# Kernel optimization log

Measured on AMD Instinct MI355X. Metric: run time of the kernel, lower is better.

## Reference

```python
import jax, jax.numpy as jnp
import numpy as np

N_HEAD = 16
RMS_EPS = 1.1920928955078125e-07  # torch float32 finfo eps (F.rms_norm default)


def _apply_rotary(x, cos, sin):
    # x: [B,T,H,D], cos/sin: [1,T,1,D/2]
    d = x.shape[-1] // 2
    x1, x2 = x[..., :d], x[..., d:]
    return jnp.concatenate([x1 * cos + x2 * sin, -x1 * sin + x2 * cos], axis=-1)


def _rms_norm(x):
    var = jnp.mean(jnp.square(x), axis=-1, keepdims=True)
    return x * jax.lax.rsqrt(var + RMS_EPS)


def setup_inputs() -> dict:
    key = jax.random.key(0)
    ks = jax.random.split(key, 5)
    B, T, C, H = 2, 2048, 1024, N_HEAD
    D = C // H
    x = jax.random.normal(ks[0], (B, T, C), dtype=jnp.float32)
    cos = jax.random.uniform(ks[1], (1, T, 1, D // 2), dtype=jnp.float32)
    sin = jax.random.uniform(ks[2], (1, T, 1, D // 2), dtype=jnp.float32)
    kv_w = jax.random.normal(ks[3], (C, C), dtype=jnp.float32) * (C ** -0.5)
    proj_w = jax.random.normal(ks[4], (C, C), dtype=jnp.float32) * (C ** -0.5)
    return {"x": x, "cos": cos, "sin": sin, "kv_w": kv_w, "proj_w": proj_w, "window_left": 1024}


def reference(x, cos, sin, kv_w, proj_w, window_left):
    B, T, C = x.shape
    H = N_HEAD
    D = C // H
    scale = D ** -0.5

    q = x.reshape(B, T, H, D)                       # no Q projection
    kv = (x @ kv_w.T).reshape(B, T, H, D)           # tied K=V projection

    q = _rms_norm(_apply_rotary(q, cos, sin))
    kv = _rms_norm(_apply_rotary(kv, cos, sin))

    # scores: [B,H,T,T]
    scores = jnp.einsum('bqhd,bkhd->bhqk', q, kv) * scale

    pos = jnp.arange(T)
    dist = pos[:, None] - pos[None, :]              # query_pos - key_pos
    allowed = (dist >= 0) & (dist <= window_left)   # causal + sliding window
    scores = jnp.where(allowed[None, None], scores, -jnp.inf)

    attn = jax.nn.softmax(scores, axis=-1)
    out = jnp.einsum('bhqk,bkhd->bqhd', attn, kv).reshape(B, T, C)
    return out @ proj_w.T
```

## Files before the change

kernel.cpp:

```cpp
#include <hip/hip_runtime.h>
#include <hip/hip_bf16.h>

using u16 = unsigned short;
typedef __attribute__((ext_vector_type(8))) short short8v;
typedef __attribute__((ext_vector_type(4))) float f32x4;

#define MFMA16(a, b, c) __builtin_amdgcn_mfma_f32_16x16x32_bf16((a), (b), (c), 0, 0, 0)

#define GLOAD16(g, l) __builtin_amdgcn_global_load_lds(                       \
    (const __attribute__((address_space(1))) void*)(const void*)(g),          \
    (__attribute__((address_space(3))) void*)(void*)(l), 16, 0, 0)

static __device__ __forceinline__ u16 f2bf(float x) {
  __hip_bfloat16 h = __float2bfloat16(x);
  return __builtin_bit_cast(u16, h);
}

__global__ __launch_bounds__(256) void cast3_f32_bf16(const float* __restrict__ a, u16* __restrict__ da,
                                                      const float* __restrict__ b, u16* __restrict__ db,
                                                      const float* __restrict__ c, u16* __restrict__ dc) {
  int bid = blockIdx.x;
  const float* s; u16* d; int i;
  if (bid < 4096)      { s = a; d = da; i = bid; }
  else if (bid < 5120) { s = b; d = db; i = bid - 4096; }
  else                 { s = c; d = dc; i = bid - 5120; }
  int idx = (i * 256 + threadIdx.x) * 4;
  float4 v = *reinterpret_cast<const float4*>(s + idx);
  ushort4 o;
  o.x = f2bf(v.x); o.y = f2bf(v.y); o.z = f2bf(v.z); o.w = f2bf(v.w);
  *reinterpret_cast<ushort4*>(d + idx) = o;
}

__global__ __launch_bounds__(256) void gemm_bt(const u16* __restrict__ A,
                                               const u16* __restrict__ Bt,
                                               float* __restrict__ C,
                                               int M, int N, int K) {
  __shared__ u16 As[4][64 * 32];
  __shared__ u16 Bs[4][128 * 32];
  unsigned flat = blockIdx.y * gridDim.x + blockIdx.x;
  unsigned nwg = gridDim.x * gridDim.y;
  unsigned swz = (flat & 7) * (nwg >> 3) + (flat >> 3);
  int bm = swz % gridDim.x, bn = swz / gridDim.x;
  int tid = threadIdx.x;
  int wid = tid >> 6, l = tid & 63, lr = l & 15, lg = l >> 4;
  int wr = wid >> 1, wc = wid & 1;

  int srow = l >> 2, scol = (l & 3) * 8;
  const u16* Ag  = A  + (size_t)(bm * 64 + wid * 16 + srow) * K + scol;
  const u16* Bg0 = Bt + (size_t)(bn * 128 + wid * 32 + srow) * K + scol;
  const u16* Bg1 = Bg0 + (size_t)16 * K;

  f32x4 acc[2][4];
#pragma unroll
  for (int m = 0; m < 2; m++)
#pragma unroll
    for (int n = 0; n < 4; n++) acc[m][n] = (f32x4){0.f, 0.f, 0.f, 0.f};

  const int NT = K >> 5;

#pragma unroll
  for (int t = 0; t < 2; t++) {
    GLOAD16(Ag + t * 32, &As[t][wid * 512]);
    GLOAD16(Bg0 + t * 32, &Bs[t][wid * 1024]);
    GLOAD16(Bg1 + t * 32, &Bs[t][wid * 1024 + 512]);
  }

  for (int t = 0; t < NT; t++) {
    int cur = t & 3;
    if (t + 2 < NT) {
      int nb = (t + 2) & 3;
      int ko = (t + 2) * 32;
      GLOAD16(Ag + ko, &As[nb][wid * 512]);
      GLOAD16(Bg0 + ko, &Bs[nb][wid * 1024]);
      GLOAD16(Bg1 + ko, &Bs[nb][wid * 1024 + 512]);
    }
    if (t + 2 < NT)      asm volatile("s_waitcnt vmcnt(6)" ::: "memory");
    else if (t + 1 < NT) asm volatile("s_waitcnt vmcnt(3)" ::: "memory");
    else                 asm volatile("s_waitcnt vmcnt(0)" ::: "memory");
    __builtin_amdgcn_s_barrier();

    short8v af[2], bfr[4];
#pragma unroll
    for (int m = 0; m < 2; m++)
      af[m] = *reinterpret_cast<const short8v*>(&As[cur][(wr * 32 + m * 16 + lr) * 32 + lg * 8]);
#pragma unroll
    for (int n = 0; n < 4; n++)
      bfr[n] = *reinterpret_cast<const short8v*>(&Bs[cur][(wc * 64 + n * 16 + lr) * 32 + lg * 8]);
    asm volatile("s_waitcnt lgkmcnt(0)" ::: "memory");
    __builtin_amdgcn_sched_barrier(0);
    __builtin_amdgcn_s_setprio(1);
#pragma unroll
    for (int m = 0; m < 2; m++)
#pragma unroll
      for (int n = 0; n < 4; n++) acc[m][n] = MFMA16(af[m], bfr[n], acc[m][n]);
    __builtin_amdgcn_s_setprio(0);
  }

#pragma unroll
  for (int m = 0; m < 2; m++)
#pragma unroll
    for (int n = 0; n < 4; n++)
#pragma unroll
      for (int r = 0; r < 4; r++) {
        int row = bm * 64 + wr * 32 + m * 16 + lg * 4 + r;
        int col = bn * 128 + wc * 64 + n * 16 + lr;
        C[(size_t)row * N + col] = acc[m][n][r];
      }
}

__global__ __launch_bounds__(256) void rope_rms(const float* __restrict__ src,
                                                u16* __restrict__ dst,
                                                const float* __restrict__ cosp,
                                                const float* __restrict__ sinp,
                                                float scale) {
  int R = blockIdx.x * 4 + (threadIdx.x >> 6);
  int l = threadIdx.x & 63;
  int h = R & 15;
  int bt = R >> 4;
  int t = bt & 2047, b = bt >> 11;

  float v = src[((size_t)R << 6) + l];
  float p = __shfl_xor(v, 32);
  float c = cosp[(t << 5) + (l & 31)];
  float s = sinp[(t << 5) + (l & 31)];
  float r = v * c + ((l < 32) ? p * s : -p * s);
  float sq = r * r;
  sq += __shfl_xor(sq, 32);
  sq += __shfl_xor(sq, 16);
  sq += __shfl_xor(sq, 8);
  sq += __shfl_xor(sq, 4);
  sq += __shfl_xor(sq, 2);
  sq += __shfl_xor(sq, 1);
  float inv = rsqrtf(sq * (1.0f / 64.0f) + 1.1920928955078125e-07f) * scale;
  dst[((((size_t)b * 16 + h) * 2048 + t) << 6) + l] = f2bf(r * inv);
}

__global__ __launch_bounds__(256) void transpose_td(const u16* __restrict__ src,
                                                    u16* __restrict__ dst) {
  __shared__ u16 Ld[64][72];
  int t0 = blockIdx.x << 6, bh = blockIdx.y;
  int tid = threadIdx.x;
#pragma unroll
  for (int i = 0; i < 2; i++) {
    int c = tid + i * 256, tr = c >> 3, sg = c & 7;
    *reinterpret_cast<short8v*>(&Ld[tr][sg * 8]) =
        *reinterpret_cast<const short8v*>(src + ((size_t)bh * 2048 + t0 + tr) * 64 + sg * 8);
  }
  __syncthreads();
#pragma unroll
  for (int i = 0; i < 2; i++) {
    int c = tid + i * 256, dr = c >> 3, sg = c & 7;
    short8v v;
#pragma unroll
    for (int j = 0; j < 8; j++) v[j] = (short)Ld[sg * 8 + j][dr];
    *reinterpret_cast<short8v*>(dst + ((size_t)bh * 64 + dr) * 2048 + t0 + sg * 8) = v;
  }
}

__global__ __launch_bounds__(256) void attn_swa(const u16* __restrict__ Q,
                                                const u16* __restrict__ KV,
                                                const u16* __restrict__ KVt,
                                                u16* __restrict__ O,
                                                const int* __restrict__ winp) {
  const int T = 2048;
  int bid = blockIdx.x;
  int bh = bid & 31;
  int qi = 31 - (bid >> 5);
  int q0 = qi << 6;
  int b = bh >> 4, h = bh & 15;
  int W = *winp;
  int tid = threadIdx.x;
  int wid = tid >> 6, l = tid & 63, lr = l & 15, lg = l >> 4;

  __shared__ u16 Kl[64][72];
  __shared__ u16 Vt[64][72];
  __shared__ u16 Pl[4][16][72];

  const u16* Qb = Q + (((size_t)bh * T + q0 + wid * 16 + lr) << 6);
  short8v aq0 = *reinterpret_cast<const short8v*>(Qb + lg * 8);
  short8v aq1 = *reinterpret_cast<const short8v*>(Qb + 32 + lg * 8);

  const short one_bf = (short)0x3F80;
  short8v vones = {one_bf, one_bf, one_bf, one_bf, one_bf, one_bf, one_bf, one_bf};

  float m_run[4], l_run[4];
  f32x4 oacc[4];
#pragma unroll
  for (int r = 0; r < 4; r++) { m_run[r] = -1e30f; l_run[r] = 0.f; }
#pragma unroll
  for (int dt = 0; dt < 4; dt++) oacc[dt] = (f32x4){0.f, 0.f, 0.f, 0.f};

  int lo = q0 - W;
  if (lo < 0) lo = 0;
  lo &= ~63;

  const u16* KVbh  = KV + (((size_t)bh * T) << 6);
  const u16* KVtbh = KVt + ((size_t)bh << 6) * T;
  int r8 = tid >> 3, sg = tid & 7;

  short8v vK0 = *reinterpret_cast<const short8v*>(KVbh + ((size_t)(lo + r8) << 6) + sg * 8);
  short8v vK1 = *reinterpret_cast<const short8v*>(KVbh + ((size_t)(lo + r8 + 32) << 6) + sg * 8);
  short8v vV0 = *reinterpret_cast<const short8v*>(KVtbh + (size_t)r8 * T + lo + sg * 8);
  short8v vV1 = *reinterpret_cast<const short8v*>(KVtbh + (size_t)(r8 + 32) * T + lo + sg * 8);

  for (int kt = lo; kt <= q0; kt += 64) {
    __syncthreads();
    *reinterpret_cast<short8v*>(&Kl[r8][sg * 8]) = vK0;
    *reinterpret_cast<short8v*>(&Kl[r8 + 32][sg * 8]) = vK1;
    *reinterpret_cast<short8v*>(&Vt[r8][sg * 8]) = vV0;
    *reinterpret_cast<short8v*>(&Vt[r8 + 32][sg * 8]) = vV1;
    __syncthreads();
    if (kt < q0) {
      vK0 = *reinterpret_cast<const short8v*>(KVbh + ((size_t)(kt + 64 + r8) << 6) + sg * 8);
      vK1 = *reinterpret_cast<const short8v*>(KVbh + ((size_t)(kt + 64 + r8 + 32) << 6) + sg * 8);
      vV0 = *reinterpret_cast<const short8v*>(KVtbh + (size_t)r8 * T + kt + 64 + sg * 8);
      vV1 = *reinterpret_cast<const short8v*>(KVtbh + (size_t)(r8 + 32) * T + kt + 64 + sg * 8);
    }

    f32x4 s[4];
    __builtin_amdgcn_s_setprio(1);
#pragma unroll
    for (int nt = 0; nt < 4; nt++) {
      s[nt] = (f32x4){0.f, 0.f, 0.f, 0.f};
      short8v b0 = *reinterpret_cast<const short8v*>(&Kl[nt * 16 + lr][lg * 8]);
      s[nt] = MFMA16(aq0, b0, s[nt]);
      short8v b1 = *reinterpret_cast<const short8v*>(&Kl[nt * 16 + lr][32 + lg * 8]);
      s[nt] = MFMA16(aq1, b1, s[nt]);
    }
    __builtin_amdgcn_s_setprio(0);

    bool edge = (kt + 63 > q0 + wid * 16) || ((q0 - kt) + wid * 16 + 15 > W);

    float al4[4];
#pragma unroll
    for (int r = 0; r < 4; r++) {
      float sv[4], mt;
      if (edge) {
        int t = q0 + wid * 16 + lg * 4 + r;
        mt = -3e38f;
#pragma unroll
        for (int nt = 0; nt < 4; nt++) {
          int k = kt + nt * 16 + lr;
          float val = ((k <= t) && (t - k <= W)) ? s[nt][r] : -3e38f;
          sv[nt] = val;
          mt = fmaxf(mt, val);
        }
      } else {
#pragma unroll
        for (int nt = 0; nt < 4; nt++) sv[nt] = s[nt][r];
        mt = fmaxf(fmaxf(sv[0], sv[1]), fmaxf(sv[2], sv[3]));
      }
      mt = fmaxf(mt, __shfl_xor(mt, 1));
      mt = fmaxf(mt, __shfl_xor(mt, 2));
      mt = fmaxf(mt, __shfl_xor(mt, 4));
      mt = fmaxf(mt, __shfl_xor(mt, 8));
      float mn = fmaxf(m_run[r], mt);
      float al = exp2f(m_run[r] - mn);
      m_run[r] = mn;
      al4[r] = al;
#pragma unroll
      for (int nt = 0; nt < 4; nt++) {
        Pl[wid][lg * 4 + r][nt * 16 + lr] = f2bf(exp2f(sv[nt] - mn));
      }
#pragma unroll
      for (int dt = 0; dt < 4; dt++) oacc[dt][r] *= al;
    }

    short8v ap0 = *reinterpret_cast<const short8v*>(&Pl[wid][lr][lg * 8]);
    short8v ap1 = *reinterpret_cast<const short8v*>(&Pl[wid][lr][32 + lg * 8]);
    f32x4 psum = (f32x4){0.f, 0.f, 0.f, 0.f};
    __builtin_amdgcn_s_setprio(1);
    psum = MFMA16(ap0, vones, psum);
    psum = MFMA16(ap1, vones, psum);
#pragma unroll
    for (int dt = 0; dt < 4; dt++) {
      short8v v0 = *reinterpret_cast<const short8v*>(&Vt[dt * 16 + lr][lg * 8]);
      oacc[dt] = MFMA16(ap0, v0, oacc[dt]);
      short8v v1 = *reinterpret_cast<const short8v*>(&Vt[dt * 16 + lr][32 + lg * 8]);
      oacc[dt] = MFMA16(ap1, v1, oacc[dt]);
    }
    __builtin_amdgcn_s_setprio(0);
#pragma unroll
    for (int r = 0; r < 4; r++) l_run[r] = l_run[r] * al4[r] + psum[r];
  }

#pragma unroll
  for (int r = 0; r < 4; r++) {
    int t = q0 + wid * 16 + lg * 4 + r;
    float inv = 1.f / l_run[r];
#pragma unroll
    for (int dt = 0; dt < 4; dt++) {
      O[(((size_t)b * T + t) << 10) + (h << 6) + dt * 16 + lr] = f2bf(oacc[dt][r] * inv);
    }
  }
}

extern "C" void kernel_launch(void* const* d_in, const int* in_sizes, int n_in,
                              void* d_out, int out_size, void* d_ws, size_t ws_size,
                              hipStream_t stream) {
  (void)in_sizes; (void)n_in; (void)out_size; (void)ws_size;
  const float* x    = (const float*)d_in[0];
  const float* cosp = (const float*)d_in[1];
  const float* sinp = (const float*)d_in[2];
  const float* kvw  = (const float*)d_in[3];
  const float* pw   = (const float*)d_in[4];
  const int*   win  = (const int*)d_in[5];

  char* w = (char*)d_ws;
  u16*   xbf   = (u16*)(w);
  u16*   kvwbf = (u16*)(w + (8u << 20));
  u16*   pwbf  = (u16*)(w + (10u << 20));
  float* kvf   = (float*)(w + (12u << 20));
  u16*   kvt   = (u16*)(w + (12u << 20));
  u16*   aout  = (u16*)(w + (20u << 20));
  u16*   kvbf  = (u16*)(w + (28u << 20));
  u16*   qbf   = xbf;

  cast3_f32_bf16<<<6144, 256, 0, stream>>>(x, xbf, kvw, kvwbf, pw, pwbf);

  gemm_bt<<<dim3(64, 8), 256, 0, stream>>>(xbf, kvwbf, kvf, 4096, 1024, 1024);

  rope_rms<<<16384, 256, 0, stream>>>(x, qbf, cosp, sinp, 0.18033688011112042f);
  rope_rms<<<16384, 256, 0, stream>>>(kvf, kvbf, cosp, sinp, 1.0f);

  transpose_td<<<dim3(32, 32), 256, 0, stream>>>(kvbf, kvt);

  attn_swa<<<1024, 256, 0, stream>>>(qbf, kvbf, kvt, aout, win);

  gemm_bt<<<dim3(64, 8), 256, 0, stream>>>(aout, pwbf, (float*)d_out, 4096, 1024, 1024);
}
```

Measured before the change: 201.4 us.

## Fuse KV rope/rmsnorm with transpose and drop online-softmax max tracking

Merges the KV rope+RMSnorm pass and the transpose kernel into one kernel that writes both the row-major and transposed bf16 KV, removing one launch and a round trip through global memory. In attention, the running max and rescaling are replaced by a fixed offset of 12 in exp2. This works because q and kv are RMS-normalized, so scaled scores are bounded (|s| ≤ 8·log2e·... ≈ 11.5). It also removes the setprio hints. The fixed offset relies on that norm bound to keep exp2 from overflowing or underflowing in bf16 and fp32.

Result: faster. 180.8 us (-10.2%).

```diff
diff --git a/kernel.cpp b/kernel.cpp
--- a/kernel.cpp
+++ b/kernel.cpp
@@ -135,16 +135,38 @@
   dst[((((size_t)b * 16 + h) * 2048 + t) << 6) + l] = f2bf(r * inv);
 }
 
-__global__ __launch_bounds__(256) void transpose_td(const u16* __restrict__ src,
-                                                    u16* __restrict__ dst) {
+__global__ __launch_bounds__(256) void rope_rms_kv(const float* __restrict__ src,
+                                                   u16* __restrict__ dst,
+                                                   u16* __restrict__ dstT,
+                                                   const float* __restrict__ cosp,
+                                                   const float* __restrict__ sinp) {
   __shared__ u16 Ld[64][72];
-  int t0 = blockIdx.x << 6, bh = blockIdx.y;
+  int t0 = blockIdx.x << 6;
+  int bh = blockIdx.y;
+  int b = bh >> 4, h = bh & 15;
   int tid = threadIdx.x;
-#pragma unroll
-  for (int i = 0; i < 2; i++) {
-    int c = tid + i * 256, tr = c >> 3, sg = c & 7;
-    *reinterpret_cast<short8v*>(&Ld[tr][sg * 8]) =
-        *reinterpret_cast<const short8v*>(src + ((size_t)bh * 2048 + t0 + tr) * 64 + sg * 8);
+  int w = tid >> 6, l = tid & 63;
+
+  float cl, sl;
+  for (int i = 0; i < 16; i++) {
+    int tt = w * 16 + i;
+    int t = t0 + tt;
+    float v = src[((((size_t)b * 2048 + t) * 16 + h) << 6) + l];
+    float p = __shfl_xor(v, 32);
+    cl = cosp[(t << 5) + (l & 31)];
+    sl = sinp[(t << 5) + (l & 31)];
+    float r = v * cl + ((l < 32) ? p * sl : -p * sl);
+    float sq = r * r;
+    sq += __shfl_xor(sq, 32);
+    sq += __shfl_xor(sq, 16);
+    sq += __shfl_xor(sq, 8);
+    sq += __shfl_xor(sq, 4);
+    sq += __shfl_xor(sq, 2);
+    sq += __shfl_xor(sq, 1);
+    float inv = rsqrtf(sq * (1.0f / 64.0f) + 1.1920928955078125e-07f);
+    u16 val = f2bf(r * inv);
+    dst[(((size_t)bh * 2048 + t) << 6) + l] = val;
+    Ld[tt][l] = val;
   }
   __syncthreads();
 #pragma unroll
@@ -153,7 +175,7 @@
     short8v v;
 #pragma unroll
     for (int j = 0; j < 8; j++) v[j] = (short)Ld[sg * 8 + j][dr];
-    *reinterpret_cast<short8v*>(dst + ((size_t)bh * 64 + dr) * 2048 + t0 + sg * 8) = v;
+    *reinterpret_cast<short8v*>(dstT + ((size_t)bh * 64 + dr) * 2048 + t0 + sg * 8) = v;
   }
 }
 
@@ -183,10 +205,10 @@
   const short one_bf = (short)0x3F80;
   short8v vones = {one_bf, one_bf, one_bf, one_bf, one_bf, one_bf, one_bf, one_bf};
 
-  float m_run[4], l_run[4];
+  float l_run[4];
   f32x4 oacc[4];
 #pragma unroll
-  for (int r = 0; r < 4; r++) { m_run[r] = -1e30f; l_run[r] = 0.f; }
+  for (int r = 0; r < 4; r++) l_run[r] = 0.f;
 #pragma unroll
   for (int dt = 0; dt < 4; dt++) oacc[dt] = (f32x4){0.f, 0.f, 0.f, 0.f};
 
@@ -218,7 +240,6 @@
     }
 
     f32x4 s[4];
-    __builtin_amdgcn_s_setprio(1);
 #pragma unroll
     for (int nt = 0; nt < 4; nt++) {
       s[nt] = (f32x4){0.f, 0.f, 0.f, 0.f};
@@ -227,49 +248,28 @@
       short8v b1 = *reinterpret_cast<const short8v*>(&Kl[nt * 16 + lr][32 + lg * 8]);
       s[nt] = MFMA16(aq1, b1, s[nt]);
     }
-    __builtin_amdgcn_s_setprio(0);
 
     bool edge = (kt + 63 > q0 + wid * 16) || ((q0 - kt) + wid * 16 + 15 > W);
-
-    float al4[4];
 #pragma unroll
     for (int r = 0; r < 4; r++) {
-      float sv[4], mt;
       if (edge) {
         int t = q0 + wid * 16 + lg * 4 + r;
-        mt = -3e38f;
 #pragma unroll
         for (int nt = 0; nt < 4; nt++) {
           int k = kt + nt * 16 + lr;
-          float val = ((k <= t) && (t - k <= W)) ? s[nt][r] : -3e38f;
-          sv[nt] = val;
-          mt = fmaxf(mt, val);
+          float val = ((k <= t) && (t - k <= W)) ? s[nt][r] : -1e30f;
+          Pl[wid][lg * 4 + r][nt * 16 + lr] = f2bf(exp2f(val - 12.f));
         }
       } else {
 #pragma unroll
-        for (int nt = 0; nt < 4; nt++) sv[nt] = s[nt][r];
-        mt = fmaxf(fmaxf(sv[0], sv[1]), fmaxf(sv[2], sv[3]));
+        for (int nt = 0; nt < 4; nt++)
+          Pl[wid][lg * 4 + r][nt * 16 + lr] = f2bf(exp2f(s[nt][r] - 12.f));
       }
-      mt = fmaxf(mt, __shfl_xor(mt, 1));
-      mt = fmaxf(mt, __shfl_xor(mt, 2));
-      mt = fmaxf(mt, __shfl_xor(mt, 4));
-      mt = fmaxf(mt, __shfl_xor(mt, 8));
-      float mn = fmaxf(m_run[r], mt);
-      float al = exp2f(m_run[r] - mn);
-      m_run[r] = mn;
-      al4[r] = al;
-#pragma unroll
-      for (int nt = 0; nt < 4; nt++) {
-        Pl[wid][lg * 4 + r][nt * 16 + lr] = f2bf(exp2f(sv[nt] - mn));
-      }
-#pragma unroll
-      for (int dt = 0; dt < 4; dt++) oacc[dt][r] *= al;
     }
 
     short8v ap0 = *reinterpret_cast<const short8v*>(&Pl[wid][lr][lg * 8]);
     short8v ap1 = *reinterpret_cast<const short8v*>(&Pl[wid][lr][32 + lg * 8]);
     f32x4 psum = (f32x4){0.f, 0.f, 0.f, 0.f};
-    __builtin_amdgcn_s_setprio(1);
     psum = MFMA16(ap0, vones, psum);
     psum = MFMA16(ap1, vones, psum);
 #pragma unroll
@@ -279,9 +279,8 @@
       short8v v1 = *reinterpret_cast<const short8v*>(&Vt[dt * 16 + lr][32 + lg * 8]);
       oacc[dt] = MFMA16(ap1, v1, oacc[dt]);
     }
-    __builtin_amdgcn_s_setprio(0);
-#pragma unroll
-    for (int r = 0; r < 4; r++) l_run[r] = l_run[r] * al4[r] + psum[r];
+#pragma unroll
+    for (int r = 0; r < 4; r++) l_run[r] += psum[r];
   }
 
 #pragma unroll
@@ -315,15 +314,14 @@
   u16*   aout  = (u16*)(w + (20u << 20));
   u16*   kvbf  = (u16*)(w + (28u << 20));
   u16*   qbf   = xbf;
+  kvt = (u16*)(w + (36u << 20));
 
   cast3_f32_bf16<<<6144, 256, 0, stream>>>(x, xbf, kvw, kvwbf, pw, pwbf);
 
   gemm_bt<<<dim3(64, 8), 256, 0, stream>>>(xbf, kvwbf, kvf, 4096, 1024, 1024);
 
   rope_rms<<<16384, 256, 0, stream>>>(x, qbf, cosp, sinp, 0.18033688011112042f);
-  rope_rms<<<16384, 256, 0, stream>>>(kvf, kvbf, cosp, sinp, 1.0f);
-
-  transpose_td<<<dim3(32, 32), 256, 0, stream>>>(kvbf, kvt);
+  rope_rms_kv<<<dim3(32, 32), 256, 0, stream>>>(kvf, kvbf, kvt, cosp, sinp);
 
   attn_swa<<<1024, 256, 0, stream>>>(qbf, kvbf, kvt, aout, win);
 
```
